# Optimization experiments

Measured on AMD Instinct MI355X. Metric: run time of the kernel, lower is better.

Reference implementation:

```python
import jax, jax.numpy as jnp
import numpy as np

S, I, CM, C, D, CZ = 128, 512, 256, 32, 32, 128
EPS = 1e-5


def setup_inputs() -> dict:
    key = jax.random.key(0)
    ks = jax.random.split(key, 7)
    x = jax.random.normal(ks[0], (1, S, I, CM), dtype=jnp.float32)
    norm_w = 1.0 + 0.1 * jax.random.normal(ks[1], (CM,), dtype=jnp.float32)
    norm_b = 0.1 * jax.random.normal(ks[2], (CM,), dtype=jnp.float32)
    Wa = jax.random.normal(ks[3], (C, CM), dtype=jnp.float32) / np.sqrt(CM)
    Wb = jax.random.normal(ks[4], (D, CM), dtype=jnp.float32) / np.sqrt(CM)
    Wo = jax.random.normal(ks[5], (CZ, C * D), dtype=jnp.float32) / np.sqrt(C * D)
    bo = 0.1 * jax.random.normal(ks[6], (CZ,), dtype=jnp.float32)
    return {"x": x, "norm_w": norm_w, "norm_b": norm_b, "Wa": Wa, "Wb": Wb, "Wo": Wo, "bo": bo}


def reference(x, norm_w, norm_b, Wa, Wb, Wo, bo):
    m = x[0]                                   # [S, I, CM] (drop leading batch dim)
    mu = jnp.mean(m, axis=-1, keepdims=True)
    var = jnp.mean((m - mu) ** 2, axis=-1, keepdims=True)
    ln = (m - mu) * jax.lax.rsqrt(var + EPS) * norm_w + norm_b
    a = jnp.einsum('sim,cm->sic', ln, Wa)      # [S, I, C]
    b = jnp.einsum('sjm,dm->sjd', ln, Wb)      # [S, J, D]
    s = a.shape[0]
    # outer product mean over S: [I, J, C, D]; flatten order is (c, d) -> c*D + d,
    # matching the reshape(chunk, C, J, D) -> permute(0,2,1,3) -> flatten in the original.
    o = jnp.einsum('sic,sjd->ijcd', a, b) * (1.0 / s)
    z = o.reshape(o.shape[0], o.shape[1], C * D) @ Wo.T + bo  # [I, J, CZ]
    return z[None]                             # [1, I, J, CZ]
```

## Files before the change

### kernel.cpp

```cpp
#include <hip/hip_runtime.h>

#define EPS 1e-5f

typedef _Float16 half8 __attribute__((ext_vector_type(8)));
typedef _Float16 half4 __attribute__((ext_vector_type(4)));
typedef float f32x4 __attribute__((ext_vector_type(4)));

#define AB_STRIDE 72
#define AB_CHUNK  (16384 * AB_STRIDE)

__device__ __forceinline__ void load16_to_lds(const void* g, void* l) {
    __builtin_amdgcn_global_load_lds((__attribute__((address_space(1))) void*)g,
                                     (__attribute__((address_space(3))) void*)l, 16, 0, 0);
}

__global__ void k_cvt(const float* __restrict__ Wo, const float* __restrict__ Wa,
                      const float* __restrict__ Wb, _Float16* __restrict__ WoH,
                      _Float16* __restrict__ WabH)
{
    int t = blockIdx.x * 256 + threadIdx.x;
    if (t < 32768) {
        int n  = t >> 8;
        int k4 = (t & 255) * 4;
        float4 v = *(const float4*)(Wo + (size_t)n * 1024 + k4);
        int c = k4 >> 5, d0 = k4 & 31;
        _Float16* dst = WoH + (size_t)n * 1024 + c;
        dst[(d0 + 0) * 32] = (_Float16)v.x;
        dst[(d0 + 1) * 32] = (_Float16)v.y;
        dst[(d0 + 2) * 32] = (_Float16)v.z;
        dst[(d0 + 3) * 32] = (_Float16)v.w;
    } else {
        int idx = (t - 32768) * 4;
        const float* src = (idx < 8192) ? (Wa + idx) : (Wb + (idx - 8192));
        float4 v = *(const float4*)src;
        half4 h;
        h[0] = (_Float16)v.x; h[1] = (_Float16)v.y; h[2] = (_Float16)v.z; h[3] = (_Float16)v.w;
        *(half4*)(WabH + idx) = h;
    }
}

__global__ __launch_bounds__(512, 6)
void k1_ln_proj(const float* __restrict__ x, const float* __restrict__ nw,
                const float* __restrict__ nb, const _Float16* __restrict__ WabH,
                _Float16* __restrict__ aT, _Float16* __restrict__ bT)
{
    __shared__ _Float16 xln[64 * 264];
    __shared__ _Float16 oT[256 * 24];

    const int tid  = threadIdx.x;
    const int lane = tid & 63;
    const int w    = tid >> 6;
    const int quad = lane >> 4;
    const int l15  = lane & 15;

    const int i0   = (blockIdx.x >> 3) * 4;
    const int s16  = blockIdx.x & 7;
    const int ck   = s16 >> 2;
    const int col0 = (s16 & 3) * 16;

    #pragma unroll
    for (int rr = 0; rr < 8; ++rr) {
        int rl = w * 8 + rr;
        int s_ = s16 * 16 + (rl >> 2);
        int i_ = i0 + (rl & 3);
        const float4* xr = (const float4*)(x + ((size_t)s_ * 512 + i_) * 256);
        float4 v = xr[lane];
        float sum = v.x + v.y + v.z + v.w;
        float ss  = v.x * v.x + v.y * v.y + v.z * v.z + v.w * v.w;
        #pragma unroll
        for (int off = 32; off > 0; off >>= 1) {
            sum += __shfl_xor(sum, off);
            ss  += __shfl_xor(ss, off);
        }
        float mu  = sum * (1.f / 256.f);
        float var = ss * (1.f / 256.f) - mu * mu;
        float rs  = rsqrtf(var + EPS);
        float4 gw = ((const float4*)nw)[lane];
        float4 gb = ((const float4*)nb)[lane];
        half4 o;
        o[0] = (_Float16)((v.x - mu) * rs * gw.x + gb.x);
        o[1] = (_Float16)((v.y - mu) * rs * gw.y + gb.y);
        o[2] = (_Float16)((v.z - mu) * rs * gw.z + gb.z);
        o[3] = (_Float16)((v.w - mu) * rs * gw.w + gb.w);
        *(half4*)(xln + rl * 264 + lane * 4) = o;
    }
    __syncthreads();

    const int mt = w & 3, ntg = w >> 2;
    f32x4 acc2[2] = {};
    #pragma unroll
    for (int kk = 0; kk < 8; ++kk) {
        half8 af = *(const half8*)(xln + (mt * 16 + l15) * 264 + kk * 32 + quad * 8);
        #pragma unroll
        for (int t = 0; t < 2; ++t) {
            half8 bf = *(const half8*)(WabH + (ntg * 32 + t * 16 + l15) * 256 + kk * 32 + quad * 8);
            acc2[t] = __builtin_amdgcn_mfma_f32_16x16x32_f16(af, bf, acc2[t], 0, 0, 0);
        }
    }

    #pragma unroll
    for (int t = 0; t < 2; ++t) {
        int c64  = ntg * 32 + t * 16 + l15;
        int base = ((c64 >= 32) ? 128 : 0) + (c64 & 31);
        int s_l  = mt * 4 + quad;
        #pragma unroll
        for (int r = 0; r < 4; ++r)
            oT[(base + r * 32) * 24 + s_l] = (_Float16)acc2[t][r];
    }
    __syncthreads();

    {
        int row = tid >> 1, h = tid & 1;
        half8 v = *(const half8*)(oT + row * 24 + h * 8);
        _Float16* dst = (row < 128) ? aT : bT;
        int grow = i0 * 32 + (row & 127);
        *(half8*)(dst + (size_t)ck * AB_CHUNK + (size_t)grow * 72 + col0 + h * 8) = v;
    }
}

__global__ __launch_bounds__(512, 4)
void k2_main(const _Float16* __restrict__ aT, const _Float16* __restrict__ bT,
             const _Float16* __restrict__ WoH, const float* __restrict__ bo,
             float* __restrict__ out)
{
    __shared__ _Float16 smem[33024];
    _Float16* sA = smem;
    _Float16* sB = smem + 256 * AB_STRIDE;
    _Float16* oL = smem;

    const int tid  = threadIdx.x;
    const int lane = tid & 63;
    const int w    = tid >> 6;
    const int quad = lane >> 4;
    const int l15  = lane & 15;
    const int wy   = w >> 1, wx = w & 1;

    const int bid    = blockIdx.x;
    const int patch  = bid >> 7, within = bid & 127;
    const int jt = ((patch & 7) << 4) | (within & 15);
    const int it = ((patch >> 3) << 3) | (within >> 4);

    const int n0 = w * 16 + l15;
    const _Float16* wp = WoH + (size_t)n0 * 1024 + quad * 8;
    half8 wreg[2][4];
    #pragma unroll
    for (int u = 0; u < 4; ++u) wreg[0][u] = *(const half8*)(wp + u * 32);
    const float bias = bo[n0];

    const char* gA = (const char*)(aT + (size_t)it * 256 * AB_STRIDE);
    const char* gB = (const char*)(bT + (size_t)jt * 128 * AB_STRIDE);

    f32x4 acc[4][4] = {};

    for (int ck = 0; ck < 2; ++ck) {
        const char* cA = gA + (size_t)ck * (AB_CHUNK * 2);
        const char* cB = gB + (size_t)ck * (AB_CHUNK * 2);
        for (int seg = w; seg < 54; seg += 8) {
            if (seg < 36) load16_to_lds(cA + seg * 1024 + lane * 16, (char*)sA + seg * 1024 + lane * 16);
            else          load16_to_lds(cB + (seg - 36) * 1024 + lane * 16, (char*)sB + (seg - 36) * 1024 + lane * 16);
        }
        __syncthreads();

        #pragma unroll
        for (int kloc = 0; kloc < 2; ++kloc) {
            half8 af[4], bf[4];
            #pragma unroll
            for (int mt = 0; mt < 4; ++mt)
                af[mt] = *(const half8*)(sA + (wy * 64 + mt * 16 + l15) * AB_STRIDE + kloc * 32 + quad * 8);
            #pragma unroll
            for (int nt = 0; nt < 4; ++nt)
                bf[nt] = *(const half8*)(sB + (wx * 64 + nt * 16 + l15) * AB_STRIDE + kloc * 32 + quad * 8);
            #pragma unroll
            for (int mt = 0; mt < 4; ++mt)
                #pragma unroll
                for (int nt = 0; nt < 4; ++nt)
                    acc[mt][nt] = __builtin_amdgcn_mfma_f32_16x16x32_f16(af[mt], bf[nt], acc[mt][nt], 0, 0, 0);
        }
        __syncthreads();
    }

    #pragma unroll
    for (int mt = 0; mt < 4; ++mt) {
        int c0     = (mt & 1) * 16 + quad * 4;
        int chunk3 = (c0 >> 3);
        int il     = wy * 2 + (mt >> 1);
        #pragma unroll
        for (int nt = 0; nt < 4; ++nt) {
            int d    = (nt & 1) * 16 + l15;
            int jl   = wx * 2 + (nt >> 1);
            int pair = il * 4 + jl;
            int cS   = (c0 & 7) + ((chunk3 ^ ((d >> 1) & 3)) << 3);
            half4 v;
            v[0] = (_Float16)(acc[mt][nt][0] * (1.f / 128.f));
            v[1] = (_Float16)(acc[mt][nt][1] * (1.f / 128.f));
            v[2] = (_Float16)(acc[mt][nt][2] * (1.f / 128.f));
            v[3] = (_Float16)(acc[mt][nt][3] * (1.f / 128.f));
            *(half4*)(oL + pair * 1032 + d * 32 + cS) = v;
        }
    }
    __syncthreads();

    f32x4 zacc[2] = {};
    #pragma unroll
    for (int g = 0; g < 8; ++g) {
        int cur = g & 1;
        if (g < 7) {
            #pragma unroll
            for (int u = 0; u < 4; ++u)
                wreg[cur ^ 1][u] = *(const half8*)(wp + (g + 1) * 128 + u * 32);
        }
        #pragma unroll
        for (int u = 0; u < 4; ++u) {
            int kk  = g * 4 + u;
            int csw = (quad ^ ((kk >> 1) & 3)) * 8;
            half8 oa0 = *(const half8*)(oL + l15 * 1032 + kk * 32 + csw);
            half8 oa1 = *(const half8*)(oL + (16 + l15) * 1032 + kk * 32 + csw);
            zacc[0] = __builtin_amdgcn_mfma_f32_16x16x32_f16(oa0, wreg[cur][u], zacc[0], 0, 0, 0);
            zacc[1] = __builtin_amdgcn_mfma_f32_16x16x32_f16(oa1, wreg[cur][u], zacc[1], 0, 0, 0);
        }
    }

    #pragma unroll
    for (int mt2 = 0; mt2 < 2; ++mt2) {
        #pragma unroll
        for (int r = 0; r < 4; ++r) {
            int il = mt2 * 4 + quad;
            int jl = r;
            out[(((size_t)(it * 8 + il)) * 512 + jt * 4 + jl) * 128 + n0 - l15 + l15] = zacc[mt2][r] + bias;
        }
    }
}

extern "C" void kernel_launch(void* const* d_in, const int* in_sizes, int n_in,
                              void* d_out, int out_size, void* d_ws, size_t ws_size,
                              hipStream_t stream)
{
    const float* x      = (const float*)d_in[0];
    const float* norm_w = (const float*)d_in[1];
    const float* norm_b = (const float*)d_in[2];
    const float* Wa     = (const float*)d_in[3];
    const float* Wb     = (const float*)d_in[4];
    const float* Wo     = (const float*)d_in[5];
    const float* bo     = (const float*)d_in[6];
    float* out = (float*)d_out;

    _Float16* aT   = (_Float16*)d_ws;
    _Float16* bT   = aT + 2 * (size_t)AB_CHUNK;
    _Float16* WoH  = bT + 2 * (size_t)AB_CHUNK;
    _Float16* WabH = WoH + 131072;

    k_cvt<<<144, 256, 0, stream>>>(Wo, Wa, Wb, WoH, WabH);
    k1_ln_proj<<<1024, 512, 0, stream>>>(x, norm_w, norm_b, WabH, aT, bT);
    k2_main<<<8192, 512, 0, stream>>>(aT, bT, WoH, bo, out);
}
```

Before: 517.1 us.

## Fuse weight conversion into LN-projection kernel and stream Wo from global in k2

Removes the separate k_cvt launch. Each k1 block now converts Wa/Wb to fp16 into shared memory itself, and the first 128 blocks transpose and convert Wo into the workspace. In k2, the register double-buffered prefetch of Wo is replaced by a direct global load inside the final GEMM loop, which lowers register pressure at the cost of exposed load latency. The k1 launch bound drops to 4 blocks per SM because of the extra shared memory, and every block redundantly converts the full Wa/Wb.

```diff
diff --git a/kernel.cpp b/kernel.cpp
--- a/kernel.cpp
+++ b/kernel.cpp
@@ -14,49 +14,50 @@
                                      (__attribute__((address_space(3))) void*)l, 16, 0, 0);
 }
 
-__global__ void k_cvt(const float* __restrict__ Wo, const float* __restrict__ Wa,
-                      const float* __restrict__ Wb, _Float16* __restrict__ WoH,
-                      _Float16* __restrict__ WabH)
+__global__ __launch_bounds__(512, 4)
+void k1_ln_proj(const float* __restrict__ x, const float* __restrict__ nw,
+                const float* __restrict__ nb, const float* __restrict__ Wa,
+                const float* __restrict__ Wb, const float* __restrict__ Wo,
+                _Float16* __restrict__ aT, _Float16* __restrict__ bT,
+                _Float16* __restrict__ WoH)
 {
-    int t = blockIdx.x * 256 + threadIdx.x;
-    if (t < 32768) {
-        int n  = t >> 8;
-        int k4 = (t & 255) * 4;
-        float4 v = *(const float4*)(Wo + (size_t)n * 1024 + k4);
-        int c = k4 >> 5, d0 = k4 & 31;
+    __shared__ _Float16 xln[64 * 264];
+    __shared__ _Float16 Wab[64 * 264];
+    __shared__ _Float16 oT[256 * 24];
+
+    const int tid  = threadIdx.x;
+    const int lane = tid & 63;
+    const int w    = tid >> 6;
+    const int quad = lane >> 4;
+    const int l15  = lane & 15;
+
+    const int i0   = (blockIdx.x >> 3) * 4;
+    const int s16  = blockIdx.x & 7;
+    const int ck   = s16 >> 2;
+    const int col0 = (s16 & 3) * 16;
+
+    if (blockIdx.x < 128 && tid < 256) {
+        int idx = blockIdx.x * 1024 + tid * 4;
+        float4 v = *(const float4*)(Wo + idx);
+        int n = idx >> 10, k = idx & 1023;
+        int c = k >> 5, d0 = k & 31;
         _Float16* dst = WoH + (size_t)n * 1024 + c;
         dst[(d0 + 0) * 32] = (_Float16)v.x;
         dst[(d0 + 1) * 32] = (_Float16)v.y;
         dst[(d0 + 2) * 32] = (_Float16)v.z;
         dst[(d0 + 3) * 32] = (_Float16)v.w;
-    } else {
-        int idx = (t - 32768) * 4;
-        const float* src = (idx < 8192) ? (Wa + idx) : (Wb + (idx - 8192));
+    }
+
+    #pragma unroll
+    for (int u = 0; u < 8; ++u) {
+        int e4 = (u * 512 + tid) * 4;
+        const float* src = (e4 < 8192) ? (Wa + e4) : (Wb + (e4 - 8192));
         float4 v = *(const float4*)src;
         half4 h;
         h[0] = (_Float16)v.x; h[1] = (_Float16)v.y; h[2] = (_Float16)v.z; h[3] = (_Float16)v.w;
-        *(half4*)(WabH + idx) = h;
-    }
-}
-
-__global__ __launch_bounds__(512, 6)
-void k1_ln_proj(const float* __restrict__ x, const float* __restrict__ nw,
-                const float* __restrict__ nb, const _Float16* __restrict__ WabH,
-                _Float16* __restrict__ aT, _Float16* __restrict__ bT)
-{
-    __shared__ _Float16 xln[64 * 264];
-    __shared__ _Float16 oT[256 * 24];
-
-    const int tid  = threadIdx.x;
-    const int lane = tid & 63;
-    const int w    = tid >> 6;
-    const int quad = lane >> 4;
-    const int l15  = lane & 15;
-
-    const int i0   = (blockIdx.x >> 3) * 4;
-    const int s16  = blockIdx.x & 7;
-    const int ck   = s16 >> 2;
-    const int col0 = (s16 & 3) * 16;
+        int r = e4 >> 8, m = e4 & 255;
+        *(half4*)(Wab + r * 264 + m) = h;
+    }
 
     #pragma unroll
     for (int rr = 0; rr < 8; ++rr) {
@@ -93,7 +94,7 @@
         half8 af = *(const half8*)(xln + (mt * 16 + l15) * 264 + kk * 32 + quad * 8);
         #pragma unroll
         for (int t = 0; t < 2; ++t) {
-            half8 bf = *(const half8*)(WabH + (ntg * 32 + t * 16 + l15) * 256 + kk * 32 + quad * 8);
+            half8 bf = *(const half8*)(Wab + (ntg * 32 + t * 16 + l15) * 264 + kk * 32 + quad * 8);
             acc2[t] = __builtin_amdgcn_mfma_f32_16x16x32_f16(af, bf, acc2[t], 0, 0, 0);
         }
     }
@@ -139,13 +140,6 @@
     const int patch  = bid >> 7, within = bid & 127;
     const int jt = ((patch & 7) << 4) | (within & 15);
     const int it = ((patch >> 3) << 3) | (within >> 4);
-
-    const int n0 = w * 16 + l15;
-    const _Float16* wp = WoH + (size_t)n0 * 1024 + quad * 8;
-    half8 wreg[2][4];
-    #pragma unroll
-    for (int u = 0; u < 4; ++u) wreg[0][u] = *(const half8*)(wp + u * 32);
-    const float bias = bo[n0];
 
     const char* gA = (const char*)(aT + (size_t)it * 256 * AB_STRIDE);
     const char* gB = (const char*)(bT + (size_t)jt * 128 * AB_STRIDE);
@@ -201,32 +195,25 @@
     __syncthreads();
 
     f32x4 zacc[2] = {};
-    #pragma unroll
-    for (int g = 0; g < 8; ++g) {
-        int cur = g & 1;
-        if (g < 7) {
-            #pragma unroll
-            for (int u = 0; u < 4; ++u)
-                wreg[cur ^ 1][u] = *(const half8*)(wp + (g + 1) * 128 + u * 32);
-        }
-        #pragma unroll
-        for (int u = 0; u < 4; ++u) {
-            int kk  = g * 4 + u;
-            int csw = (quad ^ ((kk >> 1) & 3)) * 8;
-            half8 oa0 = *(const half8*)(oL + l15 * 1032 + kk * 32 + csw);
-            half8 oa1 = *(const half8*)(oL + (16 + l15) * 1032 + kk * 32 + csw);
-            zacc[0] = __builtin_amdgcn_mfma_f32_16x16x32_f16(oa0, wreg[cur][u], zacc[0], 0, 0, 0);
-            zacc[1] = __builtin_amdgcn_mfma_f32_16x16x32_f16(oa1, wreg[cur][u], zacc[1], 0, 0, 0);
-        }
-    }
-
+    const int n0 = w * 16 + l15;
+    #pragma unroll 4
+    for (int kk = 0; kk < 32; ++kk) {
+        int csw = (quad ^ ((kk >> 1) & 3)) * 8;
+        half8 oa0 = *(const half8*)(oL + l15 * 1032 + kk * 32 + csw);
+        half8 oa1 = *(const half8*)(oL + (16 + l15) * 1032 + kk * 32 + csw);
+        half8 w0  = *(const half8*)(WoH + (size_t)n0 * 1024 + kk * 32 + quad * 8);
+        zacc[0] = __builtin_amdgcn_mfma_f32_16x16x32_f16(oa0, w0, zacc[0], 0, 0, 0);
+        zacc[1] = __builtin_amdgcn_mfma_f32_16x16x32_f16(oa1, w0, zacc[1], 0, 0, 0);
+    }
+
+    float bias = bo[n0];
     #pragma unroll
     for (int mt2 = 0; mt2 < 2; ++mt2) {
         #pragma unroll
         for (int r = 0; r < 4; ++r) {
             int il = mt2 * 4 + quad;
             int jl = r;
-            out[(((size_t)(it * 8 + il)) * 512 + jt * 4 + jl) * 128 + n0 - l15 + l15] = zacc[mt2][r] + bias;
+            out[(((size_t)(it * 8 + il)) * 512 + jt * 4 + jl) * 128 + n0] = zacc[mt2][r] + bias;
         }
     }
 }
@@ -247,9 +234,7 @@
     _Float16* aT   = (_Float16*)d_ws;
     _Float16* bT   = aT + 2 * (size_t)AB_CHUNK;
     _Float16* WoH  = bT + 2 * (size_t)AB_CHUNK;
-    _Float16* WabH = WoH + 131072;
-
-    k_cvt<<<144, 256, 0, stream>>>(Wo, Wa, Wb, WoH, WabH);
-    k1_ln_proj<<<1024, 512, 0, stream>>>(x, norm_w, norm_b, WabH, aT, bT);
+
+    k1_ln_proj<<<1024, 512, 0, stream>>>(x, norm_w, norm_b, Wa, Wb, Wo, aT, bT, WoH);
     k2_main<<<8192, 512, 0, stream>>>(aT, bT, WoH, bo, out);
 }
```

Result: faster. 496.6 us (-4.0%).
